# Kernel tuning notes

Hardware: AMD Instinct MI355X
Metric: run time of the kernel (lower is better)

## Reference

```python
import jax, jax.numpy as jnp
import numpy as np

B, L, D = 1, 2048, 4096
H, KV, HD = 32, 8, 128
ROT = 64  # head_dim * partial_rotary_factor
SCALE = HD ** -0.5
NEG = -1e9


def _apply_rope(x, cos, sin):
    # x: [B, h, L, HD]; rotate only the first ROT dims (partial rotary, rotate-half convention)
    xr, xp = x[..., :ROT], x[..., ROT:]
    x1, x2 = jnp.split(xr, 2, axis=-1)
    rotated = jnp.concatenate([-x2, x1], axis=-1)
    xr = xr * cos[None, None] + rotated * sin[None, None]
    return jnp.concatenate([xr, xp], axis=-1)


def setup_inputs() -> dict:
    key = jax.random.key(0)
    k1, k2, k3 = jax.random.split(key, 3)
    x = jax.random.normal(k1, (B, L, D), jnp.float32)
    w_qkv = jax.random.normal(k2, (D, H * HD + 2 * KV * HD), jnp.float32) * 0.02
    w_o = jax.random.normal(k3, (H * HD, D), jnp.float32) * 0.02
    # causal additive mask, broadcast over batch and heads
    causal = jnp.tril(jnp.ones((L, L), dtype=bool))
    attention_mask = jnp.where(causal, 0.0, NEG).astype(jnp.float32)[None, None]
    # rotary tables over the ROT rotary dims
    inv_freq = 1.0 / (10000.0 ** (jnp.arange(0, ROT, 2, dtype=jnp.float32) / ROT))
    t = jnp.arange(L, dtype=jnp.float32)
    freqs = jnp.outer(t, inv_freq)            # [L, ROT/2]
    emb = jnp.concatenate([freqs, freqs], -1)  # [L, ROT]
    cos, sin = jnp.cos(emb), jnp.sin(emb)
    return {"x": x, "attention_mask": attention_mask, "cos": cos, "sin": sin,
            "w_qkv": w_qkv, "w_o": w_o}


def reference(x, attention_mask, cos, sin, w_qkv, w_o):
    Bx, Lx, _ = x.shape
    qkv = x @ w_qkv                                   # [B, L, H*HD + 2*KV*HD]
    q_pos = H * HD
    kv_pos = q_pos + KV * HD
    q = qkv[:, :, :q_pos].reshape(Bx, Lx, H, HD).transpose(0, 2, 1, 3)
    k = qkv[:, :, q_pos:kv_pos].reshape(Bx, Lx, KV, HD).transpose(0, 2, 1, 3)
    v = qkv[:, :, kv_pos:].reshape(Bx, Lx, KV, HD).transpose(0, 2, 1, 3)
    q = _apply_rope(q, cos, sin)
    k = _apply_rope(k, cos, sin)
    # GQA: duplicate KV heads (as in the original module)
    n_rep = H // KV
    k = jnp.repeat(k, n_rep, axis=1)
    v = jnp.repeat(v, n_rep, axis=1)
    w = jnp.einsum("bhqd,bhkd->bhqk", q, k) * SCALE   # [B, H, L, L]
    w = jax.nn.softmax(w + attention_mask, axis=-1)
    o = jnp.einsum("bhqk,bhkd->bhqd", w, v)           # [B, H, L, HD]
    o = o.transpose(0, 2, 1, 3).reshape(Bx, Lx, H * HD)
    return o @ w_o
```

## Files before the change

### kernel.cpp

```cpp
#include <hip/hip_runtime.h>
#include <stdint.h>

typedef float f32x4 __attribute__((ext_vector_type(4)));
typedef short s16x8 __attribute__((ext_vector_type(8)));
typedef unsigned short u16x4 __attribute__((ext_vector_type(4)));

#define SCALE_F 0.08838834764831845f

__device__ __forceinline__ unsigned short f32_to_bf16(float f) {
    union { float f; unsigned int u; } v; v.f = f;
    return (unsigned short)((v.u + 0x7FFFu + ((v.u >> 16) & 1u)) >> 16);
}

__device__ __forceinline__ void gload16(const void* g, void* l) {
    __builtin_amdgcn_global_load_lds((const __attribute__((address_space(1))) unsigned int*)g,
                                     (__attribute__((address_space(3))) unsigned int*)l,
                                     16, 0, 0);
}

__global__ void k_conv_bf16(const float* __restrict__ in, unsigned short* __restrict__ out, int n4) {
    int i = blockIdx.x * 256 + threadIdx.x;
    if (i >= n4) return;
    f32x4 v = ((const f32x4*)in)[i];
    u16x4 o;
    o[0] = f32_to_bf16(v[0]); o[1] = f32_to_bf16(v[1]);
    o[2] = f32_to_bf16(v[2]); o[3] = f32_to_bf16(v[3]);
    ((u16x4*)out)[i] = o;
}

__global__ void k_transpose_bf16(const float* __restrict__ in, unsigned short* __restrict__ out,
                                 int R, int in_ld, int in_off) {
    __shared__ float tile[64][65];
    const int rb = blockIdx.y * 64, cb = blockIdx.x * 64;
    const int t = threadIdx.x;
    const int lr = t >> 4, lc4 = (t & 15) * 4;
#pragma unroll
    for (int i = 0; i < 4; ++i) {
        int r = i * 16 + lr;
        f32x4 v = *(const f32x4*)(in + (size_t)(rb + r) * in_ld + in_off + cb + lc4);
        tile[r][lc4 + 0] = v[0]; tile[r][lc4 + 1] = v[1];
        tile[r][lc4 + 2] = v[2]; tile[r][lc4 + 3] = v[3];
    }
    __syncthreads();
#pragma unroll
    for (int i = 0; i < 4; ++i) {
        int oc = cb + i * 16 + lr;
        u16x4 o;
#pragma unroll
        for (int j = 0; j < 4; ++j)
            o[j] = f32_to_bf16(tile[lc4 + j][i * 16 + lr]);
        *(u16x4*)(out + (size_t)oc * R + rb + lc4) = o;
    }
}

template<int BN>
__global__ __launch_bounds__(512, 1)
void k_gemm8p(const unsigned short* __restrict__ A, const unsigned short* __restrict__ Bt,
              float* __restrict__ C, int N, int K) {
    constexpr int BH = BN * 32;
    constexpr int NF = BN / 64;
    __shared__ __align__(16) unsigned short As[2][2][8192];
    __shared__ __align__(16) unsigned short Bs[2][2][BH];
    const int tid = threadIdx.x;
    const int lane = tid & 63, wid = tid >> 6;
    const int g = lane >> 4, l15 = lane & 15;
    const int wm = wid >> 2, wn = wid & 3;
    const int nwg = gridDim.x, bid = blockIdx.x;
    const int swz = (bid & 7) * (nwg >> 3) + (bid >> 3);
    const int ntn = N / BN;
    const int bm = swz / ntn, bn = swz - bm * ntn;
    const int brow = bm << 8, bcol = bn * BN;

    const int rS = tid >> 2;
    const int kcS = (tid & 3) ^ (rS & 3) ^ ((rS >> 2) & 3);
    const unsigned short* sA = A + (size_t)(brow + rS) * K + kcS * 8;
    const unsigned short* sB = Bt + (size_t)(bcol + rS) * K + kcS * 8;
    const int fsw = (g ^ (l15 & 3) ^ ((l15 >> 2) & 3)) * 8;

    f32x4 acc[8][NF] = {};
    const int nt = K >> 6;

    auto stA = [&](int t, int kh) {
        unsigned short* d = &As[t & 1][kh][tid * 8];
        const unsigned short* s = sA + (size_t)t * 64 + kh * 32;
        gload16(s, d);
        gload16(s + (size_t)128 * K, d + 4096);
    };
    auto stB = [&](int t, int kh) {
        unsigned short* d = &Bs[t & 1][kh][tid * 8];
        const unsigned short* s = sB + (size_t)t * 64 + kh * 32;
        gload16(s, d);
        if constexpr (BN == 256) gload16(s + (size_t)128 * K, d + 4096);
    };

    stA(0, 0); stB(0, 0); stA(0, 1); stB(0, 1);

    for (int t = 0; t < nt; ++t) {
        const int c = t & 1;
        if constexpr (BN == 256) {
            s16x8 af[4], bf[4];
            if (t + 1 < nt) { stA(t + 1, 0); asm volatile("s_waitcnt vmcnt(6)" ::: "memory"); }
            else            { asm volatile("s_waitcnt vmcnt(4)" ::: "memory"); }
            __builtin_amdgcn_s_barrier();
#pragma unroll
            for (int f = 0; f < 4; ++f)
                af[f] = *(const s16x8*)(&As[c][0][(wm * 128 + f * 16 + l15) * 32 + fsw]);
#pragma unroll
            for (int j = 0; j < 4; ++j)
                bf[j] = *(const s16x8*)(&Bs[c][0][(wn * 64 + j * 16 + l15) * 32 + fsw]);
            __builtin_amdgcn_s_setprio(1);
#pragma unroll
            for (int f = 0; f < 4; ++f)
#pragma unroll
                for (int j = 0; j < 4; ++j)
                    acc[f][j] = __builtin_amdgcn_mfma_f32_16x16x32_bf16(af[f], bf[j], acc[f][j], 0, 0, 0);
            __builtin_amdgcn_s_setprio(0);
            if (t + 1 < nt) stB(t + 1, 0);
#pragma unroll
            for (int f = 0; f < 4; ++f)
                af[f] = *(const s16x8*)(&As[c][0][(wm * 128 + 64 + f * 16 + l15) * 32 + fsw]);
            __builtin_amdgcn_s_setprio(1);
#pragma unroll
            for (int f = 0; f < 4; ++f)
#pragma unroll
                for (int j = 0; j < 4; ++j)
                    acc[4 + f][j] = __builtin_amdgcn_mfma_f32_16x16x32_bf16(af[f], bf[j], acc[4 + f][j], 0, 0, 0);
            __builtin_amdgcn_s_setprio(0);
            if (t + 1 < nt) { stA(t + 1, 1); asm volatile("s_waitcnt vmcnt(6)" ::: "memory"); }
            else            { asm volatile("s_waitcnt vmcnt(0)" ::: "memory"); }
            __builtin_amdgcn_s_barrier();
#pragma unroll
            for (int f = 0; f < 4; ++f)
                af[f] = *(const s16x8*)(&As[c][1][(wm * 128 + f * 16 + l15) * 32 + fsw]);
#pragma unroll
            for (int j = 0; j < 4; ++j)
                bf[j] = *(const s16x8*)(&Bs[c][1][(wn * 64 + j * 16 + l15) * 32 + fsw]);
            __builtin_amdgcn_s_setprio(1);
#pragma unroll
            for (int f = 0; f < 4; ++f)
#pragma unroll
                for (int j = 0; j < 4; ++j)
                    acc[f][j] = __builtin_amdgcn_mfma_f32_16x16x32_bf16(af[f], bf[j], acc[f][j], 0, 0, 0);
            __builtin_amdgcn_s_setprio(0);
            if (t + 1 < nt) stB(t + 1, 1);
#pragma unroll
            for (int f = 0; f < 4; ++f)
                af[f] = *(const s16x8*)(&As[c][1][(wm * 128 + 64 + f * 16 + l15) * 32 + fsw]);
            __builtin_amdgcn_s_setprio(1);
#pragma unroll
            for (int f = 0; f < 4; ++f)
#pragma unroll
                for (int j = 0; j < 4; ++j)
                    acc[4 + f][j] = __builtin_amdgcn_mfma_f32_16x16x32_bf16(af[f], bf[j], acc[4 + f][j], 0, 0, 0);
            __builtin_amdgcn_s_setprio(0);
        } else {
            s16x8 af[8], bf[2];
            if (t + 1 < nt) { stA(t + 1, 0); stB(t + 1, 0); asm volatile("s_waitcnt vmcnt(6)" ::: "memory"); }
            else            { asm volatile("s_waitcnt vmcnt(3)" ::: "memory"); }
            __builtin_amdgcn_s_barrier();
#pragma unroll
            for (int f = 0; f < 8; ++f)
                af[f] = *(const s16x8*)(&As[c][0][(wm * 128 + f * 16 + l15) * 32 + fsw]);
#pragma unroll
            for (int j = 0; j < 2; ++j)
                bf[j] = *(const s16x8*)(&Bs[c][0][(wn * 32 + j * 16 + l15) * 32 + fsw]);
            __builtin_amdgcn_s_setprio(1);
#pragma unroll
            for (int f = 0; f < 8; ++f)
#pragma unroll
                for (int j = 0; j < 2; ++j)
                    acc[f][j] = __builtin_amdgcn_mfma_f32_16x16x32_bf16(af[f], bf[j], acc[f][j], 0, 0, 0);
            __builtin_amdgcn_s_setprio(0);
            if (t + 1 < nt) { stA(t + 1, 1); stB(t + 1, 1); asm volatile("s_waitcnt vmcnt(6)" ::: "memory"); }
            else            { asm volatile("s_waitcnt vmcnt(0)" ::: "memory"); }
            __builtin_amdgcn_s_barrier();
#pragma unroll
            for (int f = 0; f < 8; ++f)
                af[f] = *(const s16x8*)(&As[c][1][(wm * 128 + f * 16 + l15) * 32 + fsw]);
#pragma unroll
            for (int j = 0; j < 2; ++j)
                bf[j] = *(const s16x8*)(&Bs[c][1][(wn * 32 + j * 16 + l15) * 32 + fsw]);
            __builtin_amdgcn_s_setprio(1);
#pragma unroll
            for (int f = 0; f < 8; ++f)
#pragma unroll
                for (int j = 0; j < 2; ++j)
                    acc[f][j] = __builtin_amdgcn_mfma_f32_16x16x32_bf16(af[f], bf[j], acc[f][j], 0, 0, 0);
            __builtin_amdgcn_s_setprio(0);
        }
    }

#pragma unroll
    for (int f = 0; f < 8; ++f)
#pragma unroll
        for (int j = 0; j < NF; ++j)
#pragma unroll
            for (int r = 0; r < 4; ++r)
                C[(size_t)(brow + wm * 128 + f * 16 + g * 4 + r) * N
                  + bcol + wn * (BN / 4) + j * 16 + l15] = acc[f][j][r];
}

__global__ void k_rope_pack(const float* __restrict__ qkv, const float* __restrict__ cosT,
                            const float* __restrict__ sinT, unsigned short* __restrict__ Qb,
                            unsigned short* __restrict__ Kb) {
    const int col = blockIdx.x * 256 + threadIdx.x;
    const int t = blockIdx.y;
    const float v = qkv[(size_t)t * 6144 + col];
    const int d = col & 127;
    float o = v;
    if (d < 64) {
        float c = cosT[t * 64 + d], s = sinT[t * 64 + d];
        float partner = qkv[(size_t)t * 6144 + ((d < 32) ? col + 32 : col - 32)];
        o = (d < 32) ? (v * c - partner * s) : (v * c + partner * s);
    }
    unsigned short ob = f32_to_bf16(o);
    if (col < 4096) {
        int h = col >> 7;
        Qb[((size_t)h * 2048 + t) * 128 + d] = ob;
    } else {
        int hk = (col - 4096) >> 7;
        Kb[((size_t)hk * 2048 + t) * 128 + d] = ob;
    }
}

__global__ __launch_bounds__(256, 2)
void k_attn(const unsigned short* __restrict__ Qb, const unsigned short* __restrict__ Kb,
            const unsigned short* __restrict__ Vt, unsigned short* __restrict__ Ob) {
    __shared__ __align__(16) unsigned short Ks[2][8192];
    __shared__ __align__(16) unsigned short Vs[2][8192];
    __shared__ __align__(16) unsigned short Pl[2][4][1024];
    const int h = blockIdx.y, hk = h >> 2;
    const int qbA = blockIdx.x, qbB = 31 - qbA;
    const int tid = threadIdx.x, lane = tid & 63, wid = tid >> 6;
    const int g = lane >> 4, l15 = lane & 15;
    const int qrA = qbA * 64 + wid * 16, qrB = qbB * 64 + wid * 16;
    const int swz = (l15 & 7) << 4;

    s16x8 aqA[4], aqB[4];
#pragma unroll
    for (int kc = 0; kc < 4; ++kc) {
        aqA[kc] = *(const s16x8*)(Qb + ((size_t)h * 2048 + qrA + l15) * 128 + kc * 32 + g * 8);
        aqB[kc] = *(const s16x8*)(Qb + ((size_t)h * 2048 + qrB + l15) * 128 + kc * 32 + g * 8);
    }

    const unsigned short* gK = Kb + ((size_t)hk * 2048 + (tid & 63)) * 128 + (tid >> 6) * 8;
    const unsigned short* gV = Vt + ((size_t)hk * 128 + (tid & 127)) * 2048 + (tid >> 7) * 8;

    auto stage = [&](int kb) {
        unsigned short* dK = Ks[kb & 1] + tid * 8;
        unsigned short* dV = Vs[kb & 1] + tid * 8;
        const unsigned short* sK = gK + (size_t)kb * 8192;
        const unsigned short* sV = gV + kb * 64;
#pragma unroll
        for (int i = 0; i < 4; ++i) gload16(sK + i * 32, dK + i * 2048);
#pragma unroll
        for (int i = 0; i < 4; ++i) gload16(sV + i * 16, dV + i * 2048);
    };

    f32x4 oaccA[8] = {}, oaccB[8] = {};
    float mA = -1e30f, lA = 0.f, mB = -1e30f, lB = 0.f;

    auto process = [&](const s16x8* aq, f32x4* oacc, float& mr, float& lr, int qrow0,
                       char* pw, const unsigned short* ks, const unsigned short* vs, int kb) {
        f32x4 s[4] = {};
#pragma unroll
        for (int kc = 0; kc < 4; ++kc)
#pragma unroll
            for (int kt = 0; kt < 4; ++kt) {
                s16x8 kf = *(const s16x8*)(ks + ((kc * 4 + g) * 64 + kt * 16 + l15) * 8);
                s[kt] = __builtin_amdgcn_mfma_f32_16x16x32_bf16(kf, aq[kc], s[kt], 0, 0, 0);
            }
        const int q = qrow0 + l15;
        if (kb * 64 + 63 > qrow0) {
#pragma unroll
            for (int kt = 0; kt < 4; ++kt)
#pragma unroll
                for (int r = 0; r < 4; ++r) {
                    float xv = s[kt][r] * SCALE_F;
                    s[kt][r] = (kb * 64 + kt * 16 + g * 4 + r > q) ? -3e38f : xv;
                }
        } else {
#pragma unroll
            for (int kt = 0; kt < 4; ++kt)
#pragma unroll
                for (int r = 0; r < 4; ++r) s[kt][r] *= SCALE_F;
        }
        float mx = -3e38f;
#pragma unroll
        for (int kt = 0; kt < 4; ++kt)
#pragma unroll
            for (int r = 0; r < 4; ++r) mx = fmaxf(mx, s[kt][r]);
        mx = fmaxf(mx, __shfl_xor(mx, 16));
        mx = fmaxf(mx, __shfl_xor(mx, 32));
        if (!__all(mx - mr <= 8.0f)) {
            const float mnew = fmaxf(mr, mx);
            const float scal = __expf(mr - mnew);
            mr = mnew;
            float so[4];
#pragma unroll
            for (int r = 0; r < 4; ++r) so[r] = __shfl(scal, g * 4 + r, 16);
#pragma unroll
            for (int j = 0; j < 8; ++j) {
                oacc[j][0] *= so[0]; oacc[j][1] *= so[1];
                oacc[j][2] *= so[2]; oacc[j][3] *= so[3];
            }
            lr *= scal;
        }
        float ps = 0.f;
#pragma unroll
        for (int kt = 0; kt < 4; ++kt)
#pragma unroll
            for (int r = 0; r < 4; ++r) {
                float p = __expf(s[kt][r] - mr);
                s[kt][r] = p;
                ps += p;
            }
        ps += __shfl_xor(ps, 16);
        ps += __shfl_xor(ps, 32);
        lr += ps;
#pragma unroll
        for (int kt = 0; kt < 4; ++kt) {
            unsigned int w0 = (unsigned int)f32_to_bf16(s[kt][0]) | ((unsigned int)f32_to_bf16(s[kt][1]) << 16);
            unsigned int w1 = (unsigned int)f32_to_bf16(s[kt][2]) | ((unsigned int)f32_to_bf16(s[kt][3]) << 16);
            const int b0 = (l15 * 128 + kt * 32 + g * 8) ^ swz;
            *(unsigned int*)(pw + b0) = w0;
            *(unsigned int*)(pw + b0 + 4) = w1;
        }
#pragma unroll
        for (int kc = 0; kc < 2; ++kc) {
            s16x8 pa = *(const s16x8*)(pw + ((l15 * 128 + kc * 64 + g * 16) ^ swz));
#pragma unroll
            for (int j = 0; j < 8; ++j) {
                s16x8 bv = *(const s16x8*)(vs + ((kc * 4 + g) * 128 + j * 16 + l15) * 8);
                oacc[j] = __builtin_amdgcn_mfma_f32_16x16x32_bf16(pa, bv, oacc[j], 0, 0, 0);
            }
        }
    };

    const int nkb = qbB + 1;
    stage(0);
    for (int kb = 0; kb < nkb; ++kb) {
        if (kb + 1 < nkb) {
            stage(kb + 1);
            asm volatile("s_waitcnt vmcnt(8)" ::: "memory");
        } else {
            asm volatile("s_waitcnt vmcnt(0)" ::: "memory");
        }
        __builtin_amdgcn_s_barrier();
        const unsigned short* ks = Ks[kb & 1];
        const unsigned short* vs = Vs[kb & 1];
        process(aqB, oaccB, mB, lB, qrB, (char*)Pl[1][wid], ks, vs, kb);
        if (kb <= qbA)
            process(aqA, oaccA, mA, lA, qrA, (char*)Pl[0][wid], ks, vs, kb);
        __builtin_amdgcn_s_barrier();
    }
    float liA[4], liB[4];
#pragma unroll
    for (int r = 0; r < 4; ++r) {
        liA[r] = 1.f / __shfl(lA, g * 4 + r, 16);
        liB[r] = 1.f / __shfl(lB, g * 4 + r, 16);
    }
#pragma unroll
    for (int j = 0; j < 8; ++j)
#pragma unroll
        for (int r = 0; r < 4; ++r) {
            Ob[(size_t)(qrA + g * 4 + r) * 4096 + h * 128 + j * 16 + l15] = f32_to_bf16(oaccA[j][r] * liA[r]);
            Ob[(size_t)(qrB + g * 4 + r) * 4096 + h * 128 + j * 16 + l15] = f32_to_bf16(oaccB[j][r] * liB[r]);
        }
}

extern "C" void kernel_launch(void* const* d_in, const int* in_sizes, int n_in,
                              void* d_out, int out_size, void* d_ws, size_t ws_size,
                              hipStream_t stream) {
    const float* x     = (const float*)d_in[0];
    const float* cosT  = (const float*)d_in[2];
    const float* sinT  = (const float*)d_in[3];
    const float* w_qkv = (const float*)d_in[4];
    const float* w_o   = (const float*)d_in[5];
    float* out = (float*)d_out;

    char* ws = (char*)d_ws;
    unsigned short* wT  = (unsigned short*)(ws + 0);
    float*          qkv = (float*)(ws + 50331648);
    unsigned short* Ob  = (unsigned short*)(ws + 50331648);
    unsigned short* xb  = (unsigned short*)(ws + 100663296);
    unsigned short* Qb  = xb;
    unsigned short* Kb  = (unsigned short*)(ws + 117440512);
    unsigned short* Vt  = (unsigned short*)(ws + 121634816);

    k_conv_bf16<<<8192, 256, 0, stream>>>(x, xb, 2097152);
    k_transpose_bf16<<<dim3(96, 64), 256, 0, stream>>>(w_qkv, wT, 4096, 6144, 0);
    k_gemm8p<256><<<192, 512, 0, stream>>>(xb, wT, qkv, 6144, 4096);
    k_rope_pack<<<dim3(20, 2048), 256, 0, stream>>>(qkv, cosT, sinT, Qb, Kb);
    k_transpose_bf16<<<dim3(16, 32), 256, 0, stream>>>(qkv, Vt, 2048, 6144, 5120);
    k_transpose_bf16<<<dim3(64, 64), 256, 0, stream>>>(w_o, wT, 4096, 4096, 0);
    k_attn<<<dim3(16, 32), 256, 0, stream>>>(Qb, Kb, Vt, Ob);
    k_gemm8p<128><<<256, 512, 0, stream>>>(Ob, wT, out, 4096, 4096);
}
```

Measured before the change: 394.5 us.

## Store QKV projection in bf16 and vectorize rope packing

The QKV GEMM now writes its output in bf16 instead of fp32, so the intermediate buffer is half as large. Rope/pack and the V transpose read bf16 directly, and rope processes 8 elements per thread with vector loads and stores. The change also adds setprio around the MFMA sections in attention and alters a vmcnt wait in the GEMM. Rounding QKV to bf16 happens before rope rather than after, which adds a small extra rounding error. The vmcnt change could be unsafe if it no longer covers the outstanding loads.

```diff
diff --git a/kernel.cpp b/kernel.cpp
--- a/kernel.cpp
+++ b/kernel.cpp
@@ -4,12 +4,17 @@
 typedef float f32x4 __attribute__((ext_vector_type(4)));
 typedef short s16x8 __attribute__((ext_vector_type(8)));
 typedef unsigned short u16x4 __attribute__((ext_vector_type(4)));
+typedef unsigned short u16x8 __attribute__((ext_vector_type(8)));
 
 #define SCALE_F 0.08838834764831845f
 
 __device__ __forceinline__ unsigned short f32_to_bf16(float f) {
     union { float f; unsigned int u; } v; v.f = f;
     return (unsigned short)((v.u + 0x7FFFu + ((v.u >> 16) & 1u)) >> 16);
+}
+__device__ __forceinline__ float bf16_to_f32(unsigned short h) {
+    union { unsigned int u; float f; } v; v.u = (unsigned int)h << 16;
+    return v.f;
 }
 
 __device__ __forceinline__ void gload16(const void* g, void* l) {
@@ -28,8 +33,8 @@
     ((u16x4*)out)[i] = o;
 }
 
-__global__ void k_transpose_bf16(const float* __restrict__ in, unsigned short* __restrict__ out,
-                                 int R, int in_ld, int in_off) {
+__global__ void k_transpose_f32(const float* __restrict__ in, unsigned short* __restrict__ out,
+                                int R, int in_ld, int in_off) {
     __shared__ float tile[64][65];
     const int rb = blockIdx.y * 64, cb = blockIdx.x * 64;
     const int t = threadIdx.x;
@@ -53,10 +58,35 @@
     }
 }
 
-template<int BN>
+__global__ void k_transpose_b16(const unsigned short* __restrict__ in, unsigned short* __restrict__ out,
+                                int R, int in_ld, int in_off) {
+    __shared__ unsigned short tile[64][68];
+    const int rb = blockIdx.y * 64, cb = blockIdx.x * 64;
+    const int t = threadIdx.x;
+    const int lr = t >> 4, lc4 = (t & 15) * 4;
+#pragma unroll
+    for (int i = 0; i < 4; ++i) {
+        int r = i * 16 + lr;
+        u16x4 v = *(const u16x4*)(in + (size_t)(rb + r) * in_ld + in_off + cb + lc4);
+        tile[r][lc4 + 0] = v[0]; tile[r][lc4 + 1] = v[1];
+        tile[r][lc4 + 2] = v[2]; tile[r][lc4 + 3] = v[3];
+    }
+    __syncthreads();
+#pragma unroll
+    for (int i = 0; i < 4; ++i) {
+        int oc = cb + i * 16 + lr;
+        u16x4 o;
+#pragma unroll
+        for (int j = 0; j < 4; ++j)
+            o[j] = tile[lc4 + j][i * 16 + lr];
+        *(u16x4*)(out + (size_t)oc * R + rb + lc4) = o;
+    }
+}
+
+template<int BN, typename OUT>
 __global__ __launch_bounds__(512, 1)
 void k_gemm8p(const unsigned short* __restrict__ A, const unsigned short* __restrict__ Bt,
-              float* __restrict__ C, int N, int K) {
+              OUT* __restrict__ C, int N, int K) {
     constexpr int BH = BN * 32;
     constexpr int NF = BN / 64;
     __shared__ __align__(16) unsigned short As[2][2][8192];
@@ -126,7 +156,7 @@
                 for (int j = 0; j < 4; ++j)
                     acc[4 + f][j] = __builtin_amdgcn_mfma_f32_16x16x32_bf16(af[f], bf[j], acc[4 + f][j], 0, 0, 0);
             __builtin_amdgcn_s_setprio(0);
-            if (t + 1 < nt) { stA(t + 1, 1); asm volatile("s_waitcnt vmcnt(6)" ::: "memory"); }
+            if (t + 1 < nt) { stA(t + 1, 1); asm volatile("s_waitcnt vmcnt(4)" ::: "memory"); }
             else            { asm volatile("s_waitcnt vmcnt(0)" ::: "memory"); }
             __builtin_amdgcn_s_barrier();
 #pragma unroll
@@ -195,31 +225,47 @@
 #pragma unroll
         for (int j = 0; j < NF; ++j)
 #pragma unroll
-            for (int r = 0; r < 4; ++r)
-                C[(size_t)(brow + wm * 128 + f * 16 + g * 4 + r) * N
-                  + bcol + wn * (BN / 4) + j * 16 + l15] = acc[f][j][r];
-}
-
-__global__ void k_rope_pack(const float* __restrict__ qkv, const float* __restrict__ cosT,
+            for (int r = 0; r < 4; ++r) {
+                const size_t idx = (size_t)(brow + wm * 128 + f * 16 + g * 4 + r) * N
+                                   + bcol + wn * (BN / 4) + j * 16 + l15;
+                if constexpr (sizeof(OUT) == 4) C[idx] = acc[f][j][r];
+                else                            C[idx] = f32_to_bf16(acc[f][j][r]);
+            }
+}
+
+__global__ void k_rope_pack(const unsigned short* __restrict__ qkv, const float* __restrict__ cosT,
                             const float* __restrict__ sinT, unsigned short* __restrict__ Qb,
                             unsigned short* __restrict__ Kb) {
-    const int col = blockIdx.x * 256 + threadIdx.x;
+    const int oct = blockIdx.x * 128 + threadIdx.x;
+    if (oct >= 640) return;
+    const int col = oct * 8;
     const int t = blockIdx.y;
-    const float v = qkv[(size_t)t * 6144 + col];
     const int d = col & 127;
-    float o = v;
+    u16x8 v8 = *(const u16x8*)(qkv + (size_t)t * 6144 + col);
+    u16x8 o8;
     if (d < 64) {
-        float c = cosT[t * 64 + d], s = sinT[t * 64 + d];
-        float partner = qkv[(size_t)t * 6144 + ((d < 32) ? col + 32 : col - 32)];
-        o = (d < 32) ? (v * c - partner * s) : (v * c + partner * s);
-    }
-    unsigned short ob = f32_to_bf16(o);
+        u16x8 p8 = *(const u16x8*)(qkv + (size_t)t * 6144 + (col ^ 32));
+        f32x4 c0 = *(const f32x4*)(cosT + t * 64 + d);
+        f32x4 c1 = *(const f32x4*)(cosT + t * 64 + d + 4);
+        f32x4 s0 = *(const f32x4*)(sinT + t * 64 + d);
+        f32x4 s1 = *(const f32x4*)(sinT + t * 64 + d + 4);
+        const float sgn = (d < 32) ? -1.f : 1.f;
+#pragma unroll
+        for (int j = 0; j < 8; ++j) {
+            float cc = (j < 4) ? c0[j] : c1[j - 4];
+            float ss = (j < 4) ? s0[j] : s1[j - 4];
+            float o = bf16_to_f32(v8[j]) * cc + sgn * bf16_to_f32(p8[j]) * ss;
+            o8[j] = f32_to_bf16(o);
+        }
+    } else {
+        o8 = v8;
+    }
     if (col < 4096) {
-        int h = col >> 7;
-        Qb[((size_t)h * 2048 + t) * 128 + d] = ob;
+        const int h = col >> 7;
+        *(u16x8*)(Qb + ((size_t)h * 2048 + t) * 128 + d) = o8;
     } else {
-        int hk = (col - 4096) >> 7;
-        Kb[((size_t)hk * 2048 + t) * 128 + d] = ob;
+        const int hk = (col - 4096) >> 7;
+        *(u16x8*)(Kb + ((size_t)hk * 2048 + t) * 128 + d) = o8;
     }
 }
 
@@ -263,6 +309,7 @@
     auto process = [&](const s16x8* aq, f32x4* oacc, float& mr, float& lr, int qrow0,
                        char* pw, const unsigned short* ks, const unsigned short* vs, int kb) {
         f32x4 s[4] = {};
+        __builtin_amdgcn_s_setprio(1);
 #pragma unroll
         for (int kc = 0; kc < 4; ++kc)
 #pragma unroll
@@ -270,6 +317,7 @@
                 s16x8 kf = *(const s16x8*)(ks + ((kc * 4 + g) * 64 + kt * 16 + l15) * 8);
                 s[kt] = __builtin_amdgcn_mfma_f32_16x16x32_bf16(kf, aq[kc], s[kt], 0, 0, 0);
             }
+        __builtin_amdgcn_s_setprio(0);
         const int q = qrow0 + l15;
         if (kb * 64 + 63 > qrow0) {
 #pragma unroll
@@ -326,6 +374,7 @@
             *(unsigned int*)(pw + b0) = w0;
             *(unsigned int*)(pw + b0 + 4) = w1;
         }
+        __builtin_amdgcn_s_setprio(1);
 #pragma unroll
         for (int kc = 0; kc < 2; ++kc) {
             s16x8 pa = *(const s16x8*)(pw + ((l15 * 128 + kc * 64 + g * 16) ^ swz));
@@ -335,6 +384,7 @@
                 oacc[j] = __builtin_amdgcn_mfma_f32_16x16x32_bf16(pa, bv, oacc[j], 0, 0, 0);
             }
         }
+        __builtin_amdgcn_s_setprio(0);
     };
 
     const int nkb = qbB + 1;
@@ -380,20 +430,20 @@
     float* out = (float*)d_out;
 
     char* ws = (char*)d_ws;
-    unsigned short* wT  = (unsigned short*)(ws + 0);
-    float*          qkv = (float*)(ws + 50331648);
-    unsigned short* Ob  = (unsigned short*)(ws + 50331648);
-    unsigned short* xb  = (unsigned short*)(ws + 100663296);
-    unsigned short* Qb  = xb;
-    unsigned short* Kb  = (unsigned short*)(ws + 117440512);
-    unsigned short* Vt  = (unsigned short*)(ws + 121634816);
+    unsigned short* wT   = (unsigned short*)(ws + 0);
+    unsigned short* qkvb = (unsigned short*)(ws + 50331648);
+    unsigned short* Ob   = (unsigned short*)(ws + 50331648);
+    unsigned short* xb   = (unsigned short*)(ws + 100663296);
+    unsigned short* Qb   = xb;
+    unsigned short* Kb   = (unsigned short*)(ws + 117440512);
+    unsigned short* Vt   = (unsigned short*)(ws + 121634816);
 
     k_conv_bf16<<<8192, 256, 0, stream>>>(x, xb, 2097152);
-    k_transpose_bf16<<<dim3(96, 64), 256, 0, stream>>>(w_qkv, wT, 4096, 6144, 0);
-    k_gemm8p<256><<<192, 512, 0, stream>>>(xb, wT, qkv, 6144, 4096);
-    k_rope_pack<<<dim3(20, 2048), 256, 0, stream>>>(qkv, cosT, sinT, Qb, Kb);
-    k_transpose_bf16<<<dim3(16, 32), 256, 0, stream>>>(qkv, Vt, 2048, 6144, 5120);
-    k_transpose_bf16<<<dim3(64, 64), 256, 0, stream>>>(w_o, wT, 4096, 4096, 0);
+    k_transpose_f32<<<dim3(96, 64), 256, 0, stream>>>(w_qkv, wT, 4096, 6144, 0);
+    k_gemm8p<256, unsigned short><<<192, 512, 0, stream>>>(xb, wT, qkvb, 6144, 4096);
+    k_rope_pack<<<dim3(5, 2048), 128, 0, stream>>>(qkvb, cosT, sinT, Qb, Kb);
+    k_transpose_b16<<<dim3(16, 32), 256, 0, stream>>>(qkvb, Vt, 2048, 6144, 5120);
+    k_transpose_f32<<<dim3(64, 64), 256, 0, stream>>>(w_o, wT, 4096, 4096, 0);
     k_attn<<<dim3(16, 32), 256, 0, stream>>>(Qb, Kb, Vt, Ob);
-    k_gemm8p<128><<<256, 512, 0, stream>>>(Ob, wT, out, 4096, 4096);
-}
+    k_gemm8p<128, float><<<256, 512, 0, stream>>>(Ob, wT, out, 4096, 4096);
+}
```

New measurement: 363.6 us. 7.8% less time.
